# Kernel optimization log

Measured on AMD Instinct MI355X. Metric: run time of the kernel, lower is better.

## Reference

```python
import jax, jax.numpy as jnp
import numpy as np

N = 8192
F_IN = 256
F_OUT = 64
ALPHA = 0.2  # leaky-relu negative slope
NEG_INF = -9e15


def setup_inputs() -> dict:
    key = jax.random.key(0)
    k1, k2, k3, k4 = jax.random.split(key, 4)
    h = jax.random.normal(k1, (N, F_IN), dtype=jnp.float32)
    adj = jax.random.randint(k2, (N, N), 0, 2, dtype=jnp.int32)
    W = jax.random.normal(k3, (F_IN, F_OUT), dtype=jnp.float32)
    a = jax.random.normal(k4, (2 * F_OUT, 1), dtype=jnp.float32)
    return {"h": h, "adj": adj, "W": W, "a": a}


def reference(h, adj, W, a):
    # Wh: [N, F_OUT]
    Wh = h @ W
    # Decompose a = [a1; a2]: e_ij = leakyrelu(a1^T Wh_i + a2^T Wh_j),
    # identical math to concat([Wh_i, Wh_j]) @ a without the O(N^2*2F) tensor.
    a1 = a[:F_OUT, 0]
    a2 = a[F_OUT:, 0]
    s1 = Wh @ a1  # [N]
    s2 = Wh @ a2  # [N]
    e = s1[:, None] + s2[None, :]  # [N, N]
    e = jnp.where(e > 0, e, ALPHA * e)  # leaky relu
    scores = jnp.where(adj > 0, e, NEG_INF)
    attention = jax.nn.softmax(scores, axis=1)  # [N, N]
    h_prime = attention @ Wh  # [N, F_OUT]
    return h_prime
```

## Files before the change

kernel.cpp:

```cpp
#include <hip/hip_runtime.h>

#define N 8192
#define F_IN 256
#define F_OUT 64
#define ALPHA 0.2f

typedef __attribute__((ext_vector_type(8))) short bf16x8;
typedef __attribute__((ext_vector_type(4))) float f32x4;
typedef __attribute__((ext_vector_type(4))) unsigned u32x4;
typedef __attribute__((ext_vector_type(4))) unsigned short u16x4;

__device__ __forceinline__ unsigned short f2bf(float x) {
    unsigned u = __float_as_uint(x);
    u = (u + 0x7FFFu + ((u >> 16) & 1u)) >> 16;
    return (unsigned short)u;
}
__device__ __forceinline__ float bf2f(unsigned short h) {
    return __uint_as_float((unsigned)h << 16);
}

__global__ __launch_bounds__(256) void prep_kernel(
    const float* __restrict__ W, const float* __restrict__ a,
    float* __restrict__ Wa1, float* __restrict__ Wa2,
    unsigned short* __restrict__ WbTh, unsigned short* __restrict__ WbTl) {
    __shared__ float Wl[F_IN][F_OUT + 1];
    __shared__ float al[2 * F_OUT];
    const int t = threadIdx.x;
    for (int it = 0; it < 16; ++it) {
        const int idx = it * 1024 + t * 4;
        const f32x4 v = *(const f32x4*)&W[idx];
        const int r = idx >> 6, c = idx & 63;
        Wl[r][c] = v[0]; Wl[r][c + 1] = v[1]; Wl[r][c + 2] = v[2]; Wl[r][c + 3] = v[3];
    }
    if (t < 128) al[t] = a[t];
    __syncthreads();
    float x1 = 0.f, x2 = 0.f;
#pragma unroll 8
    for (int f = 0; f < F_OUT; ++f) {
        const float wv = Wl[t][f];
        x1 += wv * al[f];
        x2 += wv * al[F_OUT + f];
    }
    Wa1[t] = x1; Wa2[t] = x2;
    const int f = t >> 2, k0 = (t & 3) * 64;
    for (int kk = 0; kk < 64; kk += 8) {
        u32x4 ph, pl;
#pragma unroll
        for (int u = 0; u < 4; ++u) {
            const float w0 = Wl[k0 + kk + 2 * u][f];
            const float w1 = Wl[k0 + kk + 2 * u + 1][f];
            const unsigned short h0 = f2bf(w0), h1 = f2bf(w1);
            const unsigned short l0 = f2bf(w0 - bf2f(h0)), l1 = f2bf(w1 - bf2f(h1));
            ph[u] = (unsigned)h0 | ((unsigned)h1 << 16);
            pl[u] = (unsigned)l0 | ((unsigned)l1 << 16);
        }
        *(u32x4*)&WbTh[f * F_IN + k0 + kk] = ph;
        *(u32x4*)&WbTl[f * F_IN + k0 + kk] = pl;
    }
}

__global__ __launch_bounds__(256) void score_kernel(
    const float* __restrict__ h, const float* __restrict__ Wa1,
    const float* __restrict__ Wa2, float* __restrict__ s1, float* __restrict__ s2) {
    __shared__ float w1l[F_IN], w2l[F_IN];
    const int t = threadIdx.x, wave = t >> 6, lane = t & 63;
    w1l[t] = Wa1[t]; w2l[t] = Wa2[t];
    __syncthreads();
    const int row0 = blockIdx.x * 16 + wave * 4;
    const f32x4 wa1 = *(const f32x4*)&w1l[lane * 4];
    const f32x4 wa2 = *(const f32x4*)&w2l[lane * 4];
#pragma unroll
    for (int r = 0; r < 4; ++r) {
        const f32x4 hv = *(const f32x4*)(h + (size_t)(row0 + r) * F_IN + lane * 4);
        float d1 = hv[0] * wa1[0] + hv[1] * wa1[1] + hv[2] * wa1[2] + hv[3] * wa1[3];
        float d2 = hv[0] * wa2[0] + hv[1] * wa2[1] + hv[2] * wa2[2] + hv[3] * wa2[3];
#pragma unroll
        for (int off = 32; off; off >>= 1) {
            d1 += __shfl_down(d1, off, 64);
            d2 += __shfl_down(d2, off, 64);
        }
        if (lane == 0) { s1[row0 + r] = d1; s2[row0 + r] = d2; }
    }
}

__global__ __launch_bounds__(64) void whT_kernel(
    const float* __restrict__ h, const unsigned short* __restrict__ WbTh,
    const unsigned short* __restrict__ WbTl, unsigned short* __restrict__ WhT) {
    const int lane = threadIdx.x;
    const int mq = lane & 15, quad = lane >> 4;
    const int i0 = blockIdx.x * 16;
    const float* hp = h + (size_t)(i0 + mq) * F_IN + quad * 8;
    const unsigned short* bph = WbTh + mq * F_IN + quad * 8;
    const unsigned short* bpl = WbTl + mq * F_IN + quad * 8;
    f32x4 acc[4] = {{0.f, 0.f, 0.f, 0.f}, {0.f, 0.f, 0.f, 0.f},
                    {0.f, 0.f, 0.f, 0.f}, {0.f, 0.f, 0.f, 0.f}};
#pragma unroll
    for (int kk = 0; kk < 8; ++kk) {
        const f32x4 h0 = *(const f32x4*)(hp + kk * 32);
        const f32x4 h1 = *(const f32x4*)(hp + kk * 32 + 4);
        bf16x8 ah, al;
#pragma unroll
        for (int u = 0; u < 8; ++u) {
            const float v = (u < 4) ? h0[u] : h1[u - 4];
            const unsigned short hi = f2bf(v);
            ah[u] = (short)hi;
            al[u] = (short)f2bf(v - bf2f(hi));
        }
#pragma unroll
        for (int nt = 0; nt < 4; ++nt) {
            const bf16x8 bh = *(const bf16x8*)(bph + nt * 16 * F_IN + kk * 32);
            const bf16x8 bl = *(const bf16x8*)(bpl + nt * 16 * F_IN + kk * 32);
            acc[nt] = __builtin_amdgcn_mfma_f32_16x16x32_bf16(ah, bh, acc[nt], 0, 0, 0);
            acc[nt] = __builtin_amdgcn_mfma_f32_16x16x32_bf16(al, bh, acc[nt], 0, 0, 0);
            acc[nt] = __builtin_amdgcn_mfma_f32_16x16x32_bf16(ah, bl, acc[nt], 0, 0, 0);
        }
    }
#pragma unroll
    for (int nt = 0; nt < 4; ++nt) {
        u16x4 o;
#pragma unroll
        for (int r = 0; r < 4; ++r) o[r] = f2bf(acc[nt][r]);
        *(u16x4*)&WhT[(size_t)(nt * 16 + mq) * N + i0 + quad * 4] = o;
    }
}

#define AROWS 16
#define MROWB 2068
__global__ __launch_bounds__(512, 4) void attn_kernel(
    const int* __restrict__ adj, const unsigned short* __restrict__ WhT,
    const float* __restrict__ s1, const float* __restrict__ s2,
    float* __restrict__ out) {
    __shared__ unsigned char maskb[AROWS * MROWB];
    __shared__ float partmax[AROWS][8];
    __shared__ float mrow[AROWS], s1l[AROWS];
    __shared__ __align__(16) float accbuf[8][AROWS][F_OUT];
    __shared__ float rowsums[8][AROWS];

    const int t = threadIdx.x, wave = t >> 6, lane = t & 63;
    const int i0 = blockIdx.x * AROWS;

    float rm[AROWS];
#pragma unroll
    for (int r = 0; r < AROWS; ++r) rm[r] = -3.0e38f;

#pragma unroll 1
    for (int u = 0; u < 2; ++u) {
        const int j = u * 4096 + t * 8;
        const f32x4 sv0 = *(const f32x4*)(s2 + j);
        const f32x4 sv1 = *(const f32x4*)(s2 + j + 4);
#pragma unroll 2
        for (int r = 0; r < AROWS; ++r) {
            const int* arow = adj + (size_t)(i0 + r) * N + j;
            const int4 a0 = *(const int4*)arow;
            const int4 a1 = *(const int4*)(arow + 4);
            unsigned m0 = (a0.x > 0 ? 1u : 0u) | (a0.y > 0 ? 2u : 0u) |
                          (a0.z > 0 ? 4u : 0u) | (a0.w > 0 ? 8u : 0u);
            unsigned m1 = (a1.x > 0 ? 1u : 0u) | (a1.y > 0 ? 2u : 0u) |
                          (a1.z > 0 ? 4u : 0u) | (a1.w > 0 ? 8u : 0u);
            float mx = -3.0e38f;
            mx = fmaxf(mx, a0.x > 0 ? sv0[0] : -3.0e38f);
            mx = fmaxf(mx, a0.y > 0 ? sv0[1] : -3.0e38f);
            mx = fmaxf(mx, a0.z > 0 ? sv0[2] : -3.0e38f);
            mx = fmaxf(mx, a0.w > 0 ? sv0[3] : -3.0e38f);
            mx = fmaxf(mx, a1.x > 0 ? sv1[0] : -3.0e38f);
            mx = fmaxf(mx, a1.y > 0 ? sv1[1] : -3.0e38f);
            mx = fmaxf(mx, a1.z > 0 ? sv1[2] : -3.0e38f);
            mx = fmaxf(mx, a1.w > 0 ? sv1[3] : -3.0e38f);
            *(unsigned short*)&maskb[r * MROWB + u * 1024 + t * 2] =
                (unsigned short)(m0 | (m1 << 8));
            rm[r] = fmaxf(rm[r], mx);
        }
    }
#pragma unroll
    for (int r = 0; r < AROWS; ++r) {
        float v = rm[r];
#pragma unroll
        for (int off = 32; off; off >>= 1) v = fmaxf(v, __shfl_down(v, off, 64));
        if (lane == 0) partmax[r][wave] = v;
    }
    __syncthreads();
    if (t < AROWS) {
        float mm = partmax[t][0];
#pragma unroll
        for (int w = 1; w < 8; ++w) mm = fmaxf(mm, partmax[t][w]);
        const float s1v = s1[i0 + t];
        const float x = s1v + mm;
        mrow[t] = fmaxf(x, ALPHA * x);
        s1l[t] = s1v;
    }
    __syncthreads();

    const int mq = lane & 15, quad = lane >> 4;
    const float s1m = s1l[mq];
    const float mr = mrow[mq];
    const int jb0 = wave * 1024;

    const float* sp = s2 + jb0 + quad * 8;
    const unsigned short* wp = WhT + (size_t)mq * N + jb0 + quad * 8;
    const unsigned char* mbp = &maskb[mq * MROWB + (jb0 >> 2) + quad * 2];

    f32x4 acc0 = {0.f, 0.f, 0.f, 0.f}, acc1 = acc0, acc2 = acc0, acc3 = acc0, accS = acc0;
    bf16x8 onesf;
#pragma unroll
    for (int u = 0; u < 8; ++u) onesf[u] = (mq == 0) ? (short)0x3F80 : (short)0;

    bf16x8 b0 = *(const bf16x8*)(wp);
    bf16x8 b1 = *(const bf16x8*)(wp + 16 * N);
    bf16x8 b2 = *(const bf16x8*)(wp + 32 * N);
    bf16x8 b3 = *(const bf16x8*)(wp + 48 * N);

    for (int c = 0; c < 32; ++c) {
        const int cn = (c + 1) & 31;
        const bf16x8 nb0 = *(const bf16x8*)(wp + cn * 32);
        const bf16x8 nb1 = *(const bf16x8*)(wp + cn * 32 + 16 * N);
        const bf16x8 nb2 = *(const bf16x8*)(wp + cn * 32 + 32 * N);
        const bf16x8 nb3 = *(const bf16x8*)(wp + cn * 32 + 48 * N);

        const unsigned mw = *(const unsigned short*)(mbp + c * 8);
        const unsigned mbyte = (mw & 0xFu) | ((mw >> 4) & 0xF0u);
        const f32x4 v0 = *(const f32x4*)(sp + c * 32);
        const f32x4 v1 = *(const f32x4*)(sp + c * 32 + 4);

        bf16x8 af;
#pragma unroll
        for (int jj = 0; jj < 8; ++jj) {
            const float s2k = (jj < 4) ? v0[jj] : v1[jj - 4];
            const float x = s1m + s2k;
            const float e = fmaxf(x, ALPHA * x);
            const float w = ((mbyte >> jj) & 1u) ? __expf(e - mr) : 0.f;
            af[jj] = (short)f2bf(w);
        }
        acc0 = __builtin_amdgcn_mfma_f32_16x16x32_bf16(af, b0, acc0, 0, 0, 0);
        acc1 = __builtin_amdgcn_mfma_f32_16x16x32_bf16(af, b1, acc1, 0, 0, 0);
        acc2 = __builtin_amdgcn_mfma_f32_16x16x32_bf16(af, b2, acc2, 0, 0, 0);
        acc3 = __builtin_amdgcn_mfma_f32_16x16x32_bf16(af, b3, acc3, 0, 0, 0);
        accS = __builtin_amdgcn_mfma_f32_16x16x32_bf16(af, onesf, accS, 0, 0, 0);
        b0 = nb0; b1 = nb1; b2 = nb2; b3 = nb3;
    }

#pragma unroll
    for (int r = 0; r < 4; ++r) {
        const int row = quad * 4 + r;
        accbuf[wave][row][0 + mq]  = acc0[r];
        accbuf[wave][row][16 + mq] = acc1[r];
        accbuf[wave][row][32 + mq] = acc2[r];
        accbuf[wave][row][48 + mq] = acc3[r];
        if (mq == 0) rowsums[wave][row] = accS[r];
    }
    __syncthreads();

    {
        const int row = t >> 5, f0 = (t & 31) * 2;
        float o0 = 0.f, o1 = 0.f, rs = 0.f;
#pragma unroll
        for (int w = 0; w < 8; ++w) {
            o0 += accbuf[w][row][f0];
            o1 += accbuf[w][row][f0 + 1];
            rs += rowsums[w][row];
        }
        const float inv = (rs > 0.f) ? 1.f / rs : 0.f;
        float2 st = {o0 * inv, o1 * inv};
        *(float2*)&out[(size_t)(i0 + row) * F_OUT + f0] = st;
    }
}

extern "C" void kernel_launch(void* const* d_in, const int* in_sizes, int n_in,
                              void* d_out, int out_size, void* d_ws, size_t ws_size,
                              hipStream_t stream) {
    const float* h   = (const float*)d_in[0];
    const int*   adj = (const int*)d_in[1];
    const float* W   = (const float*)d_in[2];
    const float* a   = (const float*)d_in[3];
    float* out = (float*)d_out;

    char* ws = (char*)d_ws;
    unsigned short* WhT = (unsigned short*)ws;
    float* s1  = (float*)(ws + (size_t)F_OUT * N * 2);
    float* s2  = s1 + N;
    float* Wa1 = s2 + N;
    float* Wa2 = Wa1 + F_IN;
    unsigned short* WbTh = (unsigned short*)(Wa2 + F_IN);
    unsigned short* WbTl = WbTh + F_OUT * F_IN;

    prep_kernel<<<1, 256, 0, stream>>>(W, a, Wa1, Wa2, WbTh, WbTl);
    score_kernel<<<N / 16, 256, 0, stream>>>(h, Wa1, Wa2, s1, s2);
    whT_kernel<<<N / 16, 64, 0, stream>>>(h, WbTh, WbTl, WhT);
    attn_kernel<<<N / AROWS, 512, 0, stream>>>(adj, WhT, s1, s2, out);
}
```

Baseline: 453.7 us.

## Split adjacency compression into separate kernel and use exp2 with prescaled scores

Moves the adjacency-to-bitmask conversion and row-max computation out of the attention kernel into a dedicated streaming kernel that writes a packed bitmask and per-row max to workspace. The attention kernel then reads compact mask bytes from global memory, drops the large shared mask buffer, and raises occupancy from 4 to 8 blocks per CU. Scores are prescaled by log2(e) so the hardware exp2 can replace expf, and bf16 conversion becomes plain truncation instead of round-to-nearest. The explicit software prefetch of WhT is removed. The trade is an extra kernel launch plus an extra global round trip for the mask, and slightly less accurate bf16 weights.

```diff
diff --git a/kernel.cpp b/kernel.cpp
--- a/kernel.cpp
+++ b/kernel.cpp
@@ -4,6 +4,7 @@
 #define F_IN 256
 #define F_OUT 64
 #define ALPHA 0.2f
+#define LOG2E 1.4426950408889634f
 
 typedef __attribute__((ext_vector_type(8))) short bf16x8;
 typedef __attribute__((ext_vector_type(4))) float f32x4;
@@ -17,6 +18,13 @@
 }
 __device__ __forceinline__ float bf2f(unsigned short h) {
     return __uint_as_float((unsigned)h << 16);
+}
+__device__ __forceinline__ float fast_exp2(float x) {
+#if __has_builtin(__builtin_amdgcn_exp2f)
+    return __builtin_amdgcn_exp2f(x);
+#else
+    return __expf(x * 0.6931471805599453f);
+#endif
 }
 
 __global__ __launch_bounds__(256) void prep_kernel(
@@ -61,7 +69,7 @@
 
 __global__ __launch_bounds__(256) void score_kernel(
     const float* __restrict__ h, const float* __restrict__ Wa1,
-    const float* __restrict__ Wa2, float* __restrict__ s1, float* __restrict__ s2) {
+    const float* __restrict__ Wa2, float* __restrict__ s1c, float* __restrict__ s2c) {
     __shared__ float w1l[F_IN], w2l[F_IN];
     const int t = threadIdx.x, wave = t >> 6, lane = t & 63;
     w1l[t] = Wa1[t]; w2l[t] = Wa2[t];
@@ -79,7 +87,7 @@
             d1 += __shfl_down(d1, off, 64);
             d2 += __shfl_down(d2, off, 64);
         }
-        if (lane == 0) { s1[row0 + r] = d1; s2[row0 + r] = d2; }
+        if (lane == 0) { s1c[row0 + r] = d1 * LOG2E; s2c[row0 + r] = d2 * LOG2E; }
     }
 }
 
@@ -124,102 +132,98 @@
     }
 }
 
+__global__ __launch_bounds__(256, 8) void compress_kernel(
+    const int* __restrict__ adj, const float* __restrict__ s2c,
+    const float* __restrict__ s1c,
+    unsigned char* __restrict__ maskbits,
+    float* __restrict__ mrowc) {
+    const int t = threadIdx.x, wave = t >> 6, lane = t & 63;
+    const int i = blockIdx.x * 4 + wave;
+    const int* __restrict__ arow = adj + (size_t)i * N;
+    unsigned char* __restrict__ mbrow = maskbits + (size_t)i * (N / 8);
+    float mx = -3.0e38f;
+
+#pragma unroll 1
+    for (int s4 = 0; s4 < 4; ++s4) {
+        int4 a0[4], a1[4];
+        f32x4 v0[4], v1[4];
+#pragma unroll
+        for (int u = 0; u < 4; ++u) {
+            const int j = (s4 * 4 + u) * 512 + lane * 8;
+            a0[u] = *(const int4*)(arow + j);
+            a1[u] = *(const int4*)(arow + j + 4);
+            v0[u] = *(const f32x4*)(s2c + j);
+            v1[u] = *(const f32x4*)(s2c + j + 4);
+        }
+#pragma unroll
+        for (int u = 0; u < 4; ++u) {
+            unsigned b = 0;
+            b |= (a0[u].x > 0) ? 0x01u : 0u;
+            b |= (a0[u].y > 0) ? 0x02u : 0u;
+            b |= (a0[u].z > 0) ? 0x04u : 0u;
+            b |= (a0[u].w > 0) ? 0x08u : 0u;
+            b |= (a1[u].x > 0) ? 0x10u : 0u;
+            b |= (a1[u].y > 0) ? 0x20u : 0u;
+            b |= (a1[u].z > 0) ? 0x40u : 0u;
+            b |= (a1[u].w > 0) ? 0x80u : 0u;
+            mx = fmaxf(mx, (a0[u].x > 0) ? v0[u][0] : -3.0e38f);
+            mx = fmaxf(mx, (a0[u].y > 0) ? v0[u][1] : -3.0e38f);
+            mx = fmaxf(mx, (a0[u].z > 0) ? v0[u][2] : -3.0e38f);
+            mx = fmaxf(mx, (a0[u].w > 0) ? v0[u][3] : -3.0e38f);
+            mx = fmaxf(mx, (a1[u].x > 0) ? v1[u][0] : -3.0e38f);
+            mx = fmaxf(mx, (a1[u].y > 0) ? v1[u][1] : -3.0e38f);
+            mx = fmaxf(mx, (a1[u].z > 0) ? v1[u][2] : -3.0e38f);
+            mx = fmaxf(mx, (a1[u].w > 0) ? v1[u][3] : -3.0e38f);
+            mbrow[(s4 * 4 + u) * 64 + lane] = (unsigned char)b;
+        }
+    }
+#pragma unroll
+    for (int off = 32; off; off >>= 1) mx = fmaxf(mx, __shfl_down(mx, off, 64));
+    if (lane == 0) {
+        const float xm = s1c[i] + mx;
+        mrowc[i] = fmaxf(xm, ALPHA * xm);
+    }
+}
+
 #define AROWS 16
-#define MROWB 2068
-__global__ __launch_bounds__(512, 4) void attn_kernel(
-    const int* __restrict__ adj, const unsigned short* __restrict__ WhT,
-    const float* __restrict__ s1, const float* __restrict__ s2,
-    float* __restrict__ out) {
-    __shared__ unsigned char maskb[AROWS * MROWB];
-    __shared__ float partmax[AROWS][8];
-    __shared__ float mrow[AROWS], s1l[AROWS];
+__global__ __launch_bounds__(512, 8) void attn_kernel(
+    const unsigned char* __restrict__ maskbits,
+    const unsigned short* __restrict__ WhT,
+    const float* __restrict__ s1c, const float* __restrict__ s2c,
+    const float* __restrict__ mrowc, float* __restrict__ out) {
+    __shared__ float s1l[AROWS], ml[AROWS];
     __shared__ __align__(16) float accbuf[8][AROWS][F_OUT];
     __shared__ float rowsums[8][AROWS];
 
     const int t = threadIdx.x, wave = t >> 6, lane = t & 63;
     const int i0 = blockIdx.x * AROWS;
-
-    float rm[AROWS];
-#pragma unroll
-    for (int r = 0; r < AROWS; ++r) rm[r] = -3.0e38f;
-
-#pragma unroll 1
-    for (int u = 0; u < 2; ++u) {
-        const int j = u * 4096 + t * 8;
-        const f32x4 sv0 = *(const f32x4*)(s2 + j);
-        const f32x4 sv1 = *(const f32x4*)(s2 + j + 4);
-#pragma unroll 2
-        for (int r = 0; r < AROWS; ++r) {
-            const int* arow = adj + (size_t)(i0 + r) * N + j;
-            const int4 a0 = *(const int4*)arow;
-            const int4 a1 = *(const int4*)(arow + 4);
-            unsigned m0 = (a0.x > 0 ? 1u : 0u) | (a0.y > 0 ? 2u : 0u) |
-                          (a0.z > 0 ? 4u : 0u) | (a0.w > 0 ? 8u : 0u);
-            unsigned m1 = (a1.x > 0 ? 1u : 0u) | (a1.y > 0 ? 2u : 0u) |
-                          (a1.z > 0 ? 4u : 0u) | (a1.w > 0 ? 8u : 0u);
-            float mx = -3.0e38f;
-            mx = fmaxf(mx, a0.x > 0 ? sv0[0] : -3.0e38f);
-            mx = fmaxf(mx, a0.y > 0 ? sv0[1] : -3.0e38f);
-            mx = fmaxf(mx, a0.z > 0 ? sv0[2] : -3.0e38f);
-            mx = fmaxf(mx, a0.w > 0 ? sv0[3] : -3.0e38f);
-            mx = fmaxf(mx, a1.x > 0 ? sv1[0] : -3.0e38f);
-            mx = fmaxf(mx, a1.y > 0 ? sv1[1] : -3.0e38f);
-            mx = fmaxf(mx, a1.z > 0 ? sv1[2] : -3.0e38f);
-            mx = fmaxf(mx, a1.w > 0 ? sv1[3] : -3.0e38f);
-            *(unsigned short*)&maskb[r * MROWB + u * 1024 + t * 2] =
-                (unsigned short)(m0 | (m1 << 8));
-            rm[r] = fmaxf(rm[r], mx);
-        }
-    }
-#pragma unroll
-    for (int r = 0; r < AROWS; ++r) {
-        float v = rm[r];
-#pragma unroll
-        for (int off = 32; off; off >>= 1) v = fmaxf(v, __shfl_down(v, off, 64));
-        if (lane == 0) partmax[r][wave] = v;
-    }
-    __syncthreads();
-    if (t < AROWS) {
-        float mm = partmax[t][0];
-#pragma unroll
-        for (int w = 1; w < 8; ++w) mm = fmaxf(mm, partmax[t][w]);
-        const float s1v = s1[i0 + t];
-        const float x = s1v + mm;
-        mrow[t] = fmaxf(x, ALPHA * x);
-        s1l[t] = s1v;
-    }
+    if (t < AROWS) { s1l[t] = s1c[i0 + t]; ml[t] = mrowc[i0 + t]; }
     __syncthreads();
 
     const int mq = lane & 15, quad = lane >> 4;
     const float s1m = s1l[mq];
-    const float mr = mrow[mq];
+    const float mr = ml[mq];
     const int jb0 = wave * 1024;
 
-    const float* sp = s2 + jb0 + quad * 8;
-    const unsigned short* wp = WhT + (size_t)mq * N + jb0 + quad * 8;
-    const unsigned char* mbp = &maskb[mq * MROWB + (jb0 >> 2) + quad * 2];
+    const unsigned char* __restrict__ mbp =
+        maskbits + (size_t)(i0 + mq) * (N / 8) + (jb0 >> 3) + quad;
+    const float* __restrict__ sp = s2c + jb0 + quad * 8;
+    const unsigned short* __restrict__ wp = WhT + (size_t)mq * N + jb0 + quad * 8;
 
     f32x4 acc0 = {0.f, 0.f, 0.f, 0.f}, acc1 = acc0, acc2 = acc0, acc3 = acc0, accS = acc0;
     bf16x8 onesf;
 #pragma unroll
     for (int u = 0; u < 8; ++u) onesf[u] = (mq == 0) ? (short)0x3F80 : (short)0;
 
-    bf16x8 b0 = *(const bf16x8*)(wp);
-    bf16x8 b1 = *(const bf16x8*)(wp + 16 * N);
-    bf16x8 b2 = *(const bf16x8*)(wp + 32 * N);
-    bf16x8 b3 = *(const bf16x8*)(wp + 48 * N);
-
     for (int c = 0; c < 32; ++c) {
-        const int cn = (c + 1) & 31;
-        const bf16x8 nb0 = *(const bf16x8*)(wp + cn * 32);
-        const bf16x8 nb1 = *(const bf16x8*)(wp + cn * 32 + 16 * N);
-        const bf16x8 nb2 = *(const bf16x8*)(wp + cn * 32 + 32 * N);
-        const bf16x8 nb3 = *(const bf16x8*)(wp + cn * 32 + 48 * N);
-
-        const unsigned mw = *(const unsigned short*)(mbp + c * 8);
-        const unsigned mbyte = (mw & 0xFu) | ((mw >> 4) & 0xF0u);
+        const unsigned mbyte = mbp[c * 4];
         const f32x4 v0 = *(const f32x4*)(sp + c * 32);
         const f32x4 v1 = *(const f32x4*)(sp + c * 32 + 4);
+        const unsigned short* wpc = wp + c * 32;
+        const bf16x8 b0 = *(const bf16x8*)(wpc);
+        const bf16x8 b1 = *(const bf16x8*)(wpc + 16 * N);
+        const bf16x8 b2 = *(const bf16x8*)(wpc + 32 * N);
+        const bf16x8 b3 = *(const bf16x8*)(wpc + 48 * N);
 
         bf16x8 af;
 #pragma unroll
@@ -227,15 +231,14 @@
             const float s2k = (jj < 4) ? v0[jj] : v1[jj - 4];
             const float x = s1m + s2k;
             const float e = fmaxf(x, ALPHA * x);
-            const float w = ((mbyte >> jj) & 1u) ? __expf(e - mr) : 0.f;
-            af[jj] = (short)f2bf(w);
+            const float w = ((mbyte >> jj) & 1u) ? fast_exp2(e - mr) : 0.f;
+            af[jj] = (short)(__float_as_uint(w) >> 16);
         }
         acc0 = __builtin_amdgcn_mfma_f32_16x16x32_bf16(af, b0, acc0, 0, 0, 0);
         acc1 = __builtin_amdgcn_mfma_f32_16x16x32_bf16(af, b1, acc1, 0, 0, 0);
         acc2 = __builtin_amdgcn_mfma_f32_16x16x32_bf16(af, b2, acc2, 0, 0, 0);
         acc3 = __builtin_amdgcn_mfma_f32_16x16x32_bf16(af, b3, acc3, 0, 0, 0);
         accS = __builtin_amdgcn_mfma_f32_16x16x32_bf16(af, onesf, accS, 0, 0, 0);
-        b0 = nb0; b1 = nb1; b2 = nb2; b3 = nb3;
     }
 
 #pragma unroll
@@ -274,16 +277,19 @@
     float* out = (float*)d_out;
 
     char* ws = (char*)d_ws;
-    unsigned short* WhT = (unsigned short*)ws;
-    float* s1  = (float*)(ws + (size_t)F_OUT * N * 2);
-    float* s2  = s1 + N;
-    float* Wa1 = s2 + N;
+    unsigned char* maskbits = (unsigned char*)ws;
+    unsigned short* WhT = (unsigned short*)(ws + (size_t)N * (N / 8));
+    float* s1c  = (float*)((char*)WhT + (size_t)F_OUT * N * 2);
+    float* s2c  = s1c + N;
+    float* mrowc = s2c + N;
+    float* Wa1 = mrowc + N;
     float* Wa2 = Wa1 + F_IN;
     unsigned short* WbTh = (unsigned short*)(Wa2 + F_IN);
     unsigned short* WbTl = WbTh + F_OUT * F_IN;
 
     prep_kernel<<<1, 256, 0, stream>>>(W, a, Wa1, Wa2, WbTh, WbTl);
-    score_kernel<<<N / 16, 256, 0, stream>>>(h, Wa1, Wa2, s1, s2);
+    score_kernel<<<N / 16, 256, 0, stream>>>(h, Wa1, Wa2, s1c, s2c);
     whT_kernel<<<N / 16, 64, 0, stream>>>(h, WbTh, WbTl, WhT);
-    attn_kernel<<<N / AROWS, 512, 0, stream>>>(adj, WhT, s1, s2, out);
-}
+    compress_kernel<<<N / 4, 256, 0, stream>>>(adj, s2c, s1c, maskbits, mrowc);
+    attn_kernel<<<N / AROWS, 512, 0, stream>>>(maskbits, WhT, s1c, s2c, mrowc, out);
+}
```

Measured after the change: 467.8 us. 1.03x slower.
